# Kernel tuning notes

Hardware: AMD Instinct MI355X
Metric: run time of the kernel (lower is better)

The kernel has to match this reference:

```python
import jax, jax.numpy as jnp
import numpy as np

B, S, D, H, KD = 4, 2048, 640, 10, 64


def setup_inputs() -> dict:
    key = jax.random.key(0)
    k0, k1, k2, k3, k4 = jax.random.split(key, 5)
    x = jax.random.normal(k0, (B, S, D), dtype=jnp.float32)
    # per-head projection weights, stacked over heads: [H, D, KD]
    Wq = jax.random.normal(k1, (H, D, KD), dtype=jnp.float32) * 0.05
    Wk = jax.random.normal(k2, (H, D, KD), dtype=jnp.float32) * 0.05
    Wv = jax.random.normal(k3, (H, D, KD), dtype=jnp.float32) * 0.05
    # output projection: [H*KD, D]
    Wo = jax.random.normal(k4, (H * KD, D), dtype=jnp.float32) * 0.05
    return {"x": x, "Wq": Wq, "Wk": Wk, "Wv": Wv, "Wo": Wo}


def reference(x, Wq, Wk, Wv, Wo):
    # Batched equivalent of the per-head Python loop:
    # each head computes q=x@Wq_h, k=x@Wk_h, v=x@Wv_h, softmax(q k^T / sqrt(KD)) @ v
    q = jnp.einsum("bsd,hdk->bhsk", x, Wq)
    k = jnp.einsum("bsd,hdk->bhsk", x, Wk)
    v = jnp.einsum("bsd,hdk->bhsk", x, Wv)
    scale = 1.0 / jnp.sqrt(jnp.asarray(KD, x.dtype))
    scores = jnp.einsum("bhsk,bhtk->bhst", q, k) * scale  # [B,H,S,S]
    attn = jax.nn.softmax(scores, axis=-1)
    z = jnp.einsum("bhst,bhtk->bhsk", attn, v)  # [B,H,S,KD]
    # concat heads along last axis (head 0 first, matching the loop order)
    z = z.transpose(0, 2, 1, 3).reshape(x.shape[0], x.shape[1], H * KD)
    return jnp.einsum("bsf,fd->bsd", z, Wo)
```

## Files before the change

### kernel.cpp

```cpp
#include <hip/hip_runtime.h>
#include <hip/hip_bf16.h>

#define B_  4
#define S_  2048
#define D_  640
#define H_  10
#define KD_ 64

typedef __attribute__((ext_vector_type(8))) short  short8;
typedef __attribute__((ext_vector_type(4))) short  short4v;
typedef __attribute__((ext_vector_type(4))) float  floatx4;
typedef __attribute__((ext_vector_type(2))) unsigned int uint2v;

static __device__ __forceinline__ short f2bf_fast(float f) {
    unsigned int u = __float_as_uint(f);
    u += 0x7fffu + ((u >> 16) & 1u);
    return (short)(u >> 16);
}
static __device__ __forceinline__ unsigned int pack2bf(float a, float b) {
    union { __hip_bfloat162 h; unsigned int u; } c;
    c.h = __float22bfloat162_rn(float2{a, b});
    return c.u;
}

static __device__ __forceinline__ void gload_lds16(const void* gp, void* lp) {
    __builtin_amdgcn_global_load_lds(
        (const __attribute__((address_space(1))) unsigned int*)gp,
        (__attribute__((address_space(3))) unsigned int*)lp, 16, 0, 0);
}

__global__ __launch_bounds__(256) void prep(
        const float* __restrict__ x,
        const float* __restrict__ Wq, const float* __restrict__ Wk,
        const float* __restrict__ Wv, const float* __restrict__ Wo,
        short* __restrict__ xb, short* __restrict__ BigT,
        short* __restrict__ WoT) {
    __shared__ float tile[32][33];
    int bid = blockIdx.x;
    if (bid < 5120) {
        int idx = (bid * 256 + threadIdx.x) * 4;
        float4 v = *(const float4*)(x + idx);
        uint2v o;
        o[0] = pack2bf(v.x, v.y);
        o[1] = pack2bf(v.z, v.w);
        *(uint2v*)(xb + idx) = o;
    } else if (bid < 6320) {
        int flat = bid - 5120;
        int bz = flat / 40, rem = flat % 40;
        int by = rem >> 1, bxx = rem & 1;
        int w = bz / 10, h = bz % 10;
        const float* W = ((w == 0) ? Wq : (w == 1) ? Wk : Wv) + h * 640 * 64;
        short* out = BigT + (w * 640 + h * 64) * 640;
        int c0 = bxx * 32;
        int r0 = by * 32;
        int tx = threadIdx.x & 31, ty = threadIdx.x >> 5;
        #pragma unroll
        for (int k = 0; k < 4; ++k)
            tile[ty + 8 * k][tx] = W[(r0 + ty + 8 * k) * 64 + c0 + tx];
        __syncthreads();
        #pragma unroll
        for (int k = 0; k < 4; ++k)
            out[(c0 + ty + 8 * k) * 640 + r0 + tx] = f2bf_fast(tile[tx][ty + 8 * k]);
    } else {
        int flat = bid - 6320;
        int c0 = (flat % 20) * 32;
        int r0 = (flat / 20) * 32;
        int tx = threadIdx.x & 31, ty = threadIdx.x >> 5;
        #pragma unroll
        for (int k = 0; k < 4; ++k)
            tile[ty + 8 * k][tx] = Wo[(r0 + ty + 8 * k) * 640 + c0 + tx];
        __syncthreads();
        #pragma unroll
        for (int k = 0; k < 4; ++k)
            WoT[(c0 + ty + 8 * k) * 640 + r0 + tx] = f2bf_fast(tile[tx][ty + 8 * k]);
    }
}


__global__ __launch_bounds__(256) void qkv_gemm(
        const short* __restrict__ X, const short* __restrict__ BigT,
        short* __restrict__ qb, short* __restrict__ kb, short* __restrict__ vtb) {
    __shared__ __align__(16) short Ab[2][128][32];
    __shared__ __align__(16) short Bb[2][128][32];

    int wave = threadIdx.x >> 6;
    int lane = threadIdx.x & 63;
    int lq = lane & 15, quad = lane >> 4;
    int wm = (wave & 1) * 64, wn = (wave >> 1) * 64;
    int tm = blockIdx.x * 128;
    int tn = blockIdx.y * 128;

    int srow = lane >> 2;
    int schunk = (lane & 3) ^ ((lane >> 3) & 3);
    const short* Asrc0 = X    + (tm + wave * 32 + srow) * 640 + schunk * 8;
    const short* Bsrc0 = BigT + (tn + wave * 32 + srow) * 640 + schunk * 8;
    const short* Asrc1 = Asrc0 + 16 * 640;
    const short* Bsrc1 = Bsrc0 + 16 * 640;

    floatx4 acc[4][4];
    for (int a = 0; a < 4; ++a)
        for (int n = 0; n < 4; ++n)
            acc[a][n] = (floatx4){0.f, 0.f, 0.f, 0.f};

    int rsw = (lq >> 1) & 3;

    gload_lds16(Asrc0, &Ab[0][wave * 32][0]);
    gload_lds16(Asrc1, &Ab[0][wave * 32 + 16][0]);
    gload_lds16(Bsrc0, &Bb[0][wave * 32][0]);
    gload_lds16(Bsrc1, &Bb[0][wave * 32 + 16][0]);

    int p = 0;
    for (int k0 = 0; k0 < 640; k0 += 32) {
        __syncthreads();
        if (k0 + 32 < 640) {
            int pn = p ^ 1;
            gload_lds16(Asrc0 + k0 + 32, &Ab[pn][wave * 32][0]);
            gload_lds16(Asrc1 + k0 + 32, &Ab[pn][wave * 32 + 16][0]);
            gload_lds16(Bsrc0 + k0 + 32, &Bb[pn][wave * 32][0]);
            gload_lds16(Bsrc1 + k0 + 32, &Bb[pn][wave * 32 + 16][0]);
        }

        short8 af[4], bf[4];
        #pragma unroll
        for (int t = 0; t < 4; ++t) {
            af[t] = *(const short8*)(&Ab[p][wm + t * 16 + lq][(quad ^ rsw) * 8]);
            bf[t] = *(const short8*)(&Bb[p][wn + t * 16 + lq][(quad ^ rsw) * 8]);
        }
        #pragma unroll
        for (int nt = 0; nt < 4; ++nt)
            #pragma unroll
            for (int mt = 0; mt < 4; ++mt)
                acc[nt][mt] = __builtin_amdgcn_mfma_f32_16x16x32_bf16(
                    bf[nt], af[mt], acc[nt][mt], 0, 0, 0);
        p ^= 1;
    }

    if (tn < 1280) {
        const float qscale = 0.18033688011112042f;
        short* dst = (tn < 640) ? qb : kb;
        float scale = (tn < 640) ? qscale : 1.0f;
        #pragma unroll
        for (int nt = 0; nt < 4; ++nt) {
            int rem = (tn + wn + nt * 16) % 640;
            int hh = rem / 64;
            int kd0 = (rem % 64) + quad * 4;
            #pragma unroll
            for (int mt = 0; mt < 4; ++mt) {
                int m = tm + wm + mt * 16 + lq;
                int b = m >> 11, s = m & 2047;
                uint2v pk;
                pk[0] = pack2bf(acc[nt][mt][0] * scale, acc[nt][mt][1] * scale);
                pk[1] = pack2bf(acc[nt][mt][2] * scale, acc[nt][mt][3] * scale);
                *(uint2v*)(dst + ((b * H_ + hh) * S_ + s) * KD_ + kd0) = pk;
            }
        }
    } else {
        #pragma unroll
        for (int nt = 0; nt < 4; ++nt) {
            int rem = (tn + wn + nt * 16) - 1280;
            int hh = rem / 64;
            int kd0 = (rem % 64) + quad * 4;
            #pragma unroll
            for (int mt = 0; mt < 4; ++mt) {
                int m = tm + wm + mt * 16 + lq;
                int b = m >> 11, s = m & 2047;
                #pragma unroll
                for (int r = 0; r < 4; ++r) {
                    vtb[((b * H_ + hh) * KD_ + kd0 + r) * S_ + s] =
                        f2bf_fast(acc[nt][mt][r]);
                }
            }
        }
    }
}

__global__ __launch_bounds__(256, 3) void attn(
        const short* __restrict__ qb, const short* __restrict__ kbuf,
        const short* __restrict__ vtb, short* __restrict__ zb) {
    __shared__ __align__(16) short Kbuf[2][64][64];
    __shared__ __align__(16) short Vbuf[2][64][64];
    __shared__ __align__(16) short Pbuf[4][2][16][72];

    int wave = threadIdx.x >> 6;
    int lane = threadIdx.x & 63;
    int lq = lane & 15, quad = lane >> 4;

    int bx = blockIdx.x;
    int xcd = bx & 7, slot = bx >> 3;
    int bh = xcd * 5 + (slot >> 4);
    int qt = slot & 15;
    int b = bh / 10, h = bh % 10;
    int q0 = qt * 128;

    const short* qp = qb + (b * H_ + h) * S_ * KD_;
    const short* kp = kbuf + (b * H_ + h) * S_ * KD_;
    const short* vp = vtb + (b * H_ + h) * KD_ * S_;

    int r8 = lane >> 3;
    int g  = (lane & 7) ^ r8;
    const short* kg0 = kp + (wave * 16 + r8) * 64 + g * 8;
    const short* kg1 = kp + (wave * 16 + 8 + r8) * 64 + g * 8;
    const short* vg0 = vp + (wave * 16 + r8) * (long)S_ + g * 8;
    const short* vg1 = vp + (wave * 16 + 8 + r8) * (long)S_ + g * 8;

    short8 qA0, qA1, qB0, qB1;
    {
        int rowA = q0 + wave * 32 + lq;
        qA0 = *(const short8*)(qp + rowA * 64 + quad * 8);
        qA1 = *(const short8*)(qp + rowA * 64 + 32 + quad * 8);
        qB0 = *(const short8*)(qp + (rowA + 16) * 64 + quad * 8);
        qB1 = *(const short8*)(qp + (rowA + 16) * 64 + 32 + quad * 8);
    }

    short8 ones;
    #pragma unroll
    for (int i = 0; i < 8; ++i) ones[i] = (short)0x3F80;

    floatx4 OA[4], OB[4];
    for (int n = 0; n < 4; ++n) {
        OA[n] = (floatx4){0.f, 0.f, 0.f, 0.f};
        OB[n] = (floatx4){0.f, 0.f, 0.f, 0.f};
    }
    floatx4 lsvA = (floatx4){0.f, 0.f, 0.f, 0.f};
    floatx4 lsvB = (floatx4){0.f, 0.f, 0.f, 0.f};

    gload_lds16(kg0, &Kbuf[0][wave * 16][0]);
    gload_lds16(kg1, &Kbuf[0][wave * 16 + 8][0]);
    gload_lds16(vg0, &Vbuf[0][wave * 16][0]);
    gload_lds16(vg1, &Vbuf[0][wave * 16 + 8][0]);

    int p = 0;
    int sw = lq & 7;

    for (int t0 = 0; t0 < S_; t0 += 64) {
        __syncthreads();

        if (t0 + 64 < S_) {
            int pn = p ^ 1;
            gload_lds16(kg0 + (t0 + 64) * 64, &Kbuf[pn][wave * 16][0]);
            gload_lds16(kg1 + (t0 + 64) * 64, &Kbuf[pn][wave * 16 + 8][0]);
            gload_lds16(vg0 + (t0 + 64),      &Vbuf[pn][wave * 16][0]);
            gload_lds16(vg1 + (t0 + 64),      &Vbuf[pn][wave * 16 + 8][0]);
        }

        const short* Kb = &Kbuf[p][0][0];
        const short* Vb = &Vbuf[p][0][0];

        floatx4 sTA[4], sTB[4];
        #pragma unroll
        for (int kblk = 0; kblk < 4; ++kblk) {
            const short* krow = Kb + (kblk * 16 + lq) * 64;
            short8 bk0 = *(const short8*)(krow + (quad ^ sw) * 8);
            short8 bk1 = *(const short8*)(krow + ((quad + 4) ^ sw) * 8);
            floatx4 zA = (floatx4){0.f, 0.f, 0.f, 0.f};
            zA = __builtin_amdgcn_mfma_f32_16x16x32_bf16(bk0, qA0, zA, 0, 0, 0);
            sTA[kblk] = __builtin_amdgcn_mfma_f32_16x16x32_bf16(bk1, qA1, zA, 0, 0, 0);
            floatx4 zB = (floatx4){0.f, 0.f, 0.f, 0.f};
            zB = __builtin_amdgcn_mfma_f32_16x16x32_bf16(bk0, qB0, zB, 0, 0, 0);
            sTB[kblk] = __builtin_amdgcn_mfma_f32_16x16x32_bf16(bk1, qB1, zB, 0, 0, 0);
        }

        #pragma unroll
        for (int kblk = 0; kblk < 4; ++kblk) {
            uint2v wa;
            wa[0] = pack2bf(__builtin_amdgcn_exp2f(sTA[kblk][0]),
                            __builtin_amdgcn_exp2f(sTA[kblk][1]));
            wa[1] = pack2bf(__builtin_amdgcn_exp2f(sTA[kblk][2]),
                            __builtin_amdgcn_exp2f(sTA[kblk][3]));
            *(uint2v*)(&Pbuf[wave][0][lq][kblk * 16 + quad * 4]) = wa;
            uint2v wb;
            wb[0] = pack2bf(__builtin_amdgcn_exp2f(sTB[kblk][0]),
                            __builtin_amdgcn_exp2f(sTB[kblk][1]));
            wb[1] = pack2bf(__builtin_amdgcn_exp2f(sTB[kblk][2]),
                            __builtin_amdgcn_exp2f(sTB[kblk][3]));
            *(uint2v*)(&Pbuf[wave][1][lq][kblk * 16 + quad * 4]) = wb;
        }

        #pragma unroll
        for (int ts = 0; ts < 2; ++ts) {
            short8 pfA = *(const short8*)(&Pbuf[wave][0][lq][ts * 32 + quad * 8]);
            short8 pfB = *(const short8*)(&Pbuf[wave][1][lq][ts * 32 + quad * 8]);
            lsvA = __builtin_amdgcn_mfma_f32_16x16x32_bf16(ones, pfA, lsvA, 0, 0, 0);
            lsvB = __builtin_amdgcn_mfma_f32_16x16x32_bf16(ones, pfB, lsvB, 0, 0, 0);
            #pragma unroll
            for (int db = 0; db < 4; ++db) {
                const short* vrow = Vb + (db * 16 + lq) * 64;
                short8 bv = *(const short8*)(vrow + ((ts * 4 + quad) ^ sw) * 8);
                OA[db] = __builtin_amdgcn_mfma_f32_16x16x32_bf16(bv, pfA, OA[db], 0, 0, 0);
                OB[db] = __builtin_amdgcn_mfma_f32_16x16x32_bf16(bv, pfB, OB[db], 0, 0, 0);
            }
        }

        p ^= 1;
    }

    float invA = 1.0f / lsvA[0];
    float invB = 1.0f / lsvB[0];

    int sA = q0 + wave * 32 + lq;
    int sB = sA + 16;
    short* zrA = zb + (b * S_ + sA) * 640 + h * 64;
    short* zrB = zb + (b * S_ + sB) * 640 + h * 64;
    #pragma unroll
    for (int db = 0; db < 4; ++db) {
        uint2v za, zv;
        za[0] = pack2bf(OA[db][0] * invA, OA[db][1] * invA);
        za[1] = pack2bf(OA[db][2] * invA, OA[db][3] * invA);
        *(uint2v*)(zrA + db * 16 + quad * 4) = za;
        zv[0] = pack2bf(OB[db][0] * invB, OB[db][1] * invB);
        zv[1] = pack2bf(OB[db][2] * invB, OB[db][3] * invB);
        *(uint2v*)(zrB + db * 16 + quad * 4) = zv;
    }
}

__global__ __launch_bounds__(256) void out_gemm(
        const short* __restrict__ Z, const short* __restrict__ WoT,
        float* __restrict__ out) {
    __shared__ __align__(16) short Ab[2][128][32];
    __shared__ __align__(16) short Bb[2][128][32];

    int wave = threadIdx.x >> 6;
    int lane = threadIdx.x & 63;
    int lq = lane & 15, quad = lane >> 4;
    int wm = (wave & 1) * 64, wn = (wave >> 1) * 64;
    int tm = blockIdx.x * 128;
    int tn = blockIdx.y * 128;

    int srow = lane >> 2;
    int schunk = (lane & 3) ^ ((lane >> 3) & 3);
    const short* Asrc0 = Z   + (tm + wave * 32 + srow) * 640 + schunk * 8;
    const short* Bsrc0 = WoT + (tn + wave * 32 + srow) * 640 + schunk * 8;
    const short* Asrc1 = Asrc0 + 16 * 640;
    const short* Bsrc1 = Bsrc0 + 16 * 640;

    floatx4 acc[4][4];
    for (int a = 0; a < 4; ++a)
        for (int n = 0; n < 4; ++n)
            acc[a][n] = (floatx4){0.f, 0.f, 0.f, 0.f};

    int rsw = (lq >> 1) & 3;

    gload_lds16(Asrc0, &Ab[0][wave * 32][0]);
    gload_lds16(Asrc1, &Ab[0][wave * 32 + 16][0]);
    gload_lds16(Bsrc0, &Bb[0][wave * 32][0]);
    gload_lds16(Bsrc1, &Bb[0][wave * 32 + 16][0]);

    int p = 0;
    for (int k0 = 0; k0 < 640; k0 += 32) {
        __syncthreads();
        if (k0 + 32 < 640) {
            int pn = p ^ 1;
            gload_lds16(Asrc0 + k0 + 32, &Ab[pn][wave * 32][0]);
            gload_lds16(Asrc1 + k0 + 32, &Ab[pn][wave * 32 + 16][0]);
            gload_lds16(Bsrc0 + k0 + 32, &Bb[pn][wave * 32][0]);
            gload_lds16(Bsrc1 + k0 + 32, &Bb[pn][wave * 32 + 16][0]);
        }

        short8 af[4], bf[4];
        #pragma unroll
        for (int t = 0; t < 4; ++t) {
            af[t] = *(const short8*)(&Ab[p][wm + t * 16 + lq][(quad ^ rsw) * 8]);
            bf[t] = *(const short8*)(&Bb[p][wn + t * 16 + lq][(quad ^ rsw) * 8]);
        }
        #pragma unroll
        for (int nt = 0; nt < 4; ++nt)
            #pragma unroll
            for (int mt = 0; mt < 4; ++mt)
                acc[nt][mt] = __builtin_amdgcn_mfma_f32_16x16x32_bf16(
                    bf[nt], af[mt], acc[nt][mt], 0, 0, 0);
        p ^= 1;
    }

    #pragma unroll
    for (int nt = 0; nt < 4; ++nt) {
        int n0 = tn + wn + nt * 16 + quad * 4;
        #pragma unroll
        for (int mt = 0; mt < 4; ++mt) {
            int m = tm + wm + mt * 16 + lq;
            float4 v4 = make_float4(acc[nt][mt][0], acc[nt][mt][1],
                                    acc[nt][mt][2], acc[nt][mt][3]);
            *(float4*)(out + m * 640 + n0) = v4;
        }
    }
}

extern "C" void kernel_launch(void* const* d_in, const int* in_sizes, int n_in,
                              void* d_out, int out_size, void* d_ws, size_t ws_size,
                              hipStream_t stream) {
    const float* x  = (const float*)d_in[0];
    const float* Wq = (const float*)d_in[1];
    const float* Wk = (const float*)d_in[2];
    const float* Wv = (const float*)d_in[3];
    const float* Wo = (const float*)d_in[4];
    float* out = (float*)d_out;

    char* ws = (char*)d_ws;
    short* BigT = (short*)(ws);
    short* WoT  = (short*)(ws + 2457600);
    short* xb   = (short*)(ws + 3276800);
    short* qb   = (short*)(ws + 13762560);
    short* kb   = (short*)(ws + 24248320);
    short* vtb  = (short*)(ws + 34734080);
    short* zb   = xb;

    prep<<<dim3(6720), dim3(256), 0, stream>>>(x, Wq, Wk, Wv, Wo, xb, BigT, WoT);
    qkv_gemm<<<dim3(64, 15), dim3(256), 0, stream>>>(xb, BigT, qb, kb, vtb);
    attn<<<dim3(640), dim3(256), 0, stream>>>(qb, kb, vtb, zb);
    out_gemm<<<dim3(64, 5), dim3(256), 0, stream>>>(zb, WoT, out);
}
```

Before: 196.0 us.

## Fold Q scale into weights, sum softmax row in VALU, widen x conversion

The Q scale factor is now applied while transposing Wq to bf16 in prep, which removes the per-element multiply in the QKV GEMM epilogue. In attention, the softmax denominator is accumulated from fp32 exp values in registers and reduced with cross-lane shuffles, replacing two extra MFMAs per half-tile that summed with a ones vector. The x-to-bf16 conversion handles 8 elements per thread, halving the block count. zb now gets its own workspace region instead of aliasing xb. The row sum now comes from unrounded fp32 exps rather than bf16-rounded P, and it adds VALU adds and shuffles.

```diff
diff --git a/kernel.cpp b/kernel.cpp
--- a/kernel.cpp
+++ b/kernel.cpp
@@ -11,6 +11,7 @@
 typedef __attribute__((ext_vector_type(4))) short  short4v;
 typedef __attribute__((ext_vector_type(4))) float  floatx4;
 typedef __attribute__((ext_vector_type(2))) unsigned int uint2v;
+typedef __attribute__((ext_vector_type(4))) unsigned int uint4v;
 
 static __device__ __forceinline__ short f2bf_fast(float f) {
     unsigned int u = __float_as_uint(f);
@@ -37,19 +38,24 @@
         short* __restrict__ WoT) {
     __shared__ float tile[32][33];
     int bid = blockIdx.x;
-    if (bid < 5120) {
-        int idx = (bid * 256 + threadIdx.x) * 4;
-        float4 v = *(const float4*)(x + idx);
-        uint2v o;
-        o[0] = pack2bf(v.x, v.y);
-        o[1] = pack2bf(v.z, v.w);
-        *(uint2v*)(xb + idx) = o;
-    } else if (bid < 6320) {
-        int flat = bid - 5120;
+    if (bid < 2560) {
+        int idx = (bid * 256 + threadIdx.x) * 8;
+        float4 v0 = *(const float4*)(x + idx);
+        float4 v1 = *(const float4*)(x + idx + 4);
+        uint4v o;
+        o[0] = pack2bf(v0.x, v0.y);
+        o[1] = pack2bf(v0.z, v0.w);
+        o[2] = pack2bf(v1.x, v1.y);
+        o[3] = pack2bf(v1.z, v1.w);
+        *(uint4v*)(xb + idx) = o;
+    } else if (bid < 3760) {
+        int flat = bid - 2560;
         int bz = flat / 40, rem = flat % 40;
         int by = rem >> 1, bxx = rem & 1;
         int w = bz / 10, h = bz % 10;
         const float* W = ((w == 0) ? Wq : (w == 1) ? Wk : Wv) + h * 640 * 64;
+        const float qscale = 0.18033688011112042f;
+        float scale = (w == 0) ? qscale : 1.0f;
         short* out = BigT + (w * 640 + h * 64) * 640;
         int c0 = bxx * 32;
         int r0 = by * 32;
@@ -60,9 +66,10 @@
         __syncthreads();
         #pragma unroll
         for (int k = 0; k < 4; ++k)
-            out[(c0 + ty + 8 * k) * 640 + r0 + tx] = f2bf_fast(tile[tx][ty + 8 * k]);
+            out[(c0 + ty + 8 * k) * 640 + r0 + tx] =
+                f2bf_fast(tile[tx][ty + 8 * k] * scale);
     } else {
-        int flat = bid - 6320;
+        int flat = bid - 3760;
         int c0 = (flat % 20) * 32;
         int r0 = (flat / 20) * 32;
         int tx = threadIdx.x & 31, ty = threadIdx.x >> 5;
@@ -136,9 +143,7 @@
     }
 
     if (tn < 1280) {
-        const float qscale = 0.18033688011112042f;
         short* dst = (tn < 640) ? qb : kb;
-        float scale = (tn < 640) ? qscale : 1.0f;
         #pragma unroll
         for (int nt = 0; nt < 4; ++nt) {
             int rem = (tn + wn + nt * 16) % 640;
@@ -149,8 +154,8 @@
                 int m = tm + wm + mt * 16 + lq;
                 int b = m >> 11, s = m & 2047;
                 uint2v pk;
-                pk[0] = pack2bf(acc[nt][mt][0] * scale, acc[nt][mt][1] * scale);
-                pk[1] = pack2bf(acc[nt][mt][2] * scale, acc[nt][mt][3] * scale);
+                pk[0] = pack2bf(acc[nt][mt][0], acc[nt][mt][1]);
+                pk[1] = pack2bf(acc[nt][mt][2], acc[nt][mt][3]);
                 *(uint2v*)(dst + ((b * H_ + hh) * S_ + s) * KD_ + kd0) = pk;
             }
         }
@@ -212,17 +217,12 @@
         qB1 = *(const short8*)(qp + (rowA + 16) * 64 + 32 + quad * 8);
     }
 
-    short8 ones;
-    #pragma unroll
-    for (int i = 0; i < 8; ++i) ones[i] = (short)0x3F80;
-
     floatx4 OA[4], OB[4];
     for (int n = 0; n < 4; ++n) {
         OA[n] = (floatx4){0.f, 0.f, 0.f, 0.f};
         OB[n] = (floatx4){0.f, 0.f, 0.f, 0.f};
     }
-    floatx4 lsvA = (floatx4){0.f, 0.f, 0.f, 0.f};
-    floatx4 lsvB = (floatx4){0.f, 0.f, 0.f, 0.f};
+    float lsA = 0.f, lsB = 0.f;
 
     gload_lds16(kg0, &Kbuf[0][wave * 16][0]);
     gload_lds16(kg1, &Kbuf[0][wave * 16 + 8][0]);
@@ -262,17 +262,19 @@
 
         #pragma unroll
         for (int kblk = 0; kblk < 4; ++kblk) {
-            uint2v wa;
-            wa[0] = pack2bf(__builtin_amdgcn_exp2f(sTA[kblk][0]),
-                            __builtin_amdgcn_exp2f(sTA[kblk][1]));
-            wa[1] = pack2bf(__builtin_amdgcn_exp2f(sTA[kblk][2]),
-                            __builtin_amdgcn_exp2f(sTA[kblk][3]));
+            float a0 = __builtin_amdgcn_exp2f(sTA[kblk][0]);
+            float a1 = __builtin_amdgcn_exp2f(sTA[kblk][1]);
+            float a2 = __builtin_amdgcn_exp2f(sTA[kblk][2]);
+            float a3 = __builtin_amdgcn_exp2f(sTA[kblk][3]);
+            lsA += (a0 + a1) + (a2 + a3);
+            uint2v wa; wa[0] = pack2bf(a0, a1); wa[1] = pack2bf(a2, a3);
             *(uint2v*)(&Pbuf[wave][0][lq][kblk * 16 + quad * 4]) = wa;
-            uint2v wb;
-            wb[0] = pack2bf(__builtin_amdgcn_exp2f(sTB[kblk][0]),
-                            __builtin_amdgcn_exp2f(sTB[kblk][1]));
-            wb[1] = pack2bf(__builtin_amdgcn_exp2f(sTB[kblk][2]),
-                            __builtin_amdgcn_exp2f(sTB[kblk][3]));
+            float b0 = __builtin_amdgcn_exp2f(sTB[kblk][0]);
+            float b1 = __builtin_amdgcn_exp2f(sTB[kblk][1]);
+            float b2 = __builtin_amdgcn_exp2f(sTB[kblk][2]);
+            float b3 = __builtin_amdgcn_exp2f(sTB[kblk][3]);
+            lsB += (b0 + b1) + (b2 + b3);
+            uint2v wb; wb[0] = pack2bf(b0, b1); wb[1] = pack2bf(b2, b3);
             *(uint2v*)(&Pbuf[wave][1][lq][kblk * 16 + quad * 4]) = wb;
         }
 
@@ -280,8 +282,6 @@
         for (int ts = 0; ts < 2; ++ts) {
             short8 pfA = *(const short8*)(&Pbuf[wave][0][lq][ts * 32 + quad * 8]);
             short8 pfB = *(const short8*)(&Pbuf[wave][1][lq][ts * 32 + quad * 8]);
-            lsvA = __builtin_amdgcn_mfma_f32_16x16x32_bf16(ones, pfA, lsvA, 0, 0, 0);
-            lsvB = __builtin_amdgcn_mfma_f32_16x16x32_bf16(ones, pfB, lsvB, 0, 0, 0);
             #pragma unroll
             for (int db = 0; db < 4; ++db) {
                 const short* vrow = Vb + (db * 16 + lq) * 64;
@@ -294,8 +294,11 @@
         p ^= 1;
     }
 
-    float invA = 1.0f / lsvA[0];
-    float invB = 1.0f / lsvB[0];
+    lsA += __shfl_xor(lsA, 16);
+    lsA += __shfl_xor(lsA, 32);
+    lsB += __shfl_xor(lsB, 16);
+    lsB += __shfl_xor(lsB, 32);
+    float invA = 1.0f / lsA, invB = 1.0f / lsB;
 
     int sA = q0 + wave * 32 + lq;
     int sB = sA + 16;
@@ -401,9 +404,9 @@
     short* qb   = (short*)(ws + 13762560);
     short* kb   = (short*)(ws + 24248320);
     short* vtb  = (short*)(ws + 34734080);
-    short* zb   = xb;
-
-    prep<<<dim3(6720), dim3(256), 0, stream>>>(x, Wq, Wk, Wv, Wo, xb, BigT, WoT);
+    short* zb   = (short*)(ws + 45219840);
+
+    prep<<<dim3(4160), dim3(256), 0, stream>>>(x, Wq, Wk, Wv, Wo, xb, BigT, WoT);
     qkv_gemm<<<dim3(64, 15), dim3(256), 0, stream>>>(xb, BigT, qb, kb, vtb);
     attn<<<dim3(640), dim3(256), 0, stream>>>(qb, kb, vtb, zb);
     out_gemm<<<dim3(64, 5), dim3(256), 0, stream>>>(zb, WoT, out);
```

New measurement: 194.5 us. Within noise of the previous version (-0.8%).
